# Kernel optimization log

Measured on AMD Instinct MI355X. Metric: run time of the kernel, lower is better.

## Reference

```python
import jax, jax.numpy as jnp
import numpy as np

N, L, E_Q, E_TOTAL, H, FORECAST = 4, 2048, 512, 512, 8, 8
E_HEAD = E_TOTAL // H
DT = 1.0
NEG = -1e30


def setup_inputs() -> dict:
    rng = jax.random.key(0)
    ks = jax.random.split(rng, 8)
    inv = 1.0 / np.sqrt(E_Q)
    return {
        "query": jax.random.normal(ks[0], (N, L, E_Q), jnp.float32),
        "key": jax.random.normal(ks[1], (N, L, E_Q), jnp.float32),
        "value": jax.random.normal(ks[2], (N, L, E_Q), jnp.float32),
        "Wqkv": jax.random.normal(ks[3], (E_Q, 3 * E_TOTAL), jnp.float32) * inv,
        "bqkv": jnp.zeros((3 * E_TOTAL,), jnp.float32),
        "Wo": jax.random.normal(ks[4], (E_TOTAL, E_Q), jnp.float32) * (1.0 / np.sqrt(E_TOTAL)),
        "bo": jnp.zeros((E_Q,), jnp.float32),
        "Xi": jax.random.normal(ks[5], (H, E_HEAD, E_HEAD), jnp.float32) * 0.02,
    }


def reference(query, key, value, Wqkv, bqkv, Wo, bo, Xi):
    # NOTE: original forward projects `query` into q,k,v (key/value args unused).
    b, s, _ = query.shape
    qkv = query @ Wqkv + bqkv                      # [b, s, 3E]
    q, k, v = jnp.split(qkv, 3, axis=-1)
    split_heads = lambda t: t.reshape(b, s, H, E_HEAD).transpose(0, 2, 1, 3)  # [b,H,s,h]
    q, k, v = split_heads(q), split_heads(k), split_heads(v)
    # causal SDPA
    scale = 1.0 / np.sqrt(E_HEAD)
    scores = jnp.einsum('bhqd,bhkd->bhqk', q, k) * scale
    causal = jnp.tril(jnp.ones((s, s), bool))
    scores = jnp.where(causal, scores, NEG)
    probs = jax.nn.softmax(scores, axis=-1)
    attn = jnp.einsum('bhqk,bhkd->bhqd', probs, v)  # [b,H,s,h]
    # per-head SINDy linear dynamics, strict symmetry -> skew-symmetric A
    A = Xi - jnp.swapaxes(Xi, -1, -2)               # [H,h,h]

    def step(x, _):
        x2 = x + DT * jnp.einsum('bhsd,hde->bhse', x, A)
        return x2, x2

    _, ys = jax.lax.scan(step, attn, None, length=FORECAST)  # [n,b,H,s,h]
    roll = jnp.transpose(ys, (1, 0, 3, 2, 4)).reshape(b, FORECAST, s, E_TOTAL)
    return roll @ Wo + bo                            # [b, n, s, E_q]
```

## Files before the change

kernel.cpp:

```cpp
#include <hip/hip_runtime.h>
#include <math.h>


#define NEGV -1e30f

typedef __bf16 bf16_t;
typedef __bf16 bf16x4 __attribute__((ext_vector_type(4)));
typedef __bf16 bf16x8 __attribute__((ext_vector_type(8)));
typedef float f32x4 __attribute__((ext_vector_type(4)));

#define MFMA(a, b, c) __builtin_amdgcn_mfma_f32_16x16x32_bf16((a), (b), (c), 0, 0, 0)

#define QSCALE 0.18033688011112042f

__device__ __forceinline__ bf16x8* swz_ptr(bf16_t* base, int r, int cb) {
  return (bf16x8*)((char*)base + r * 128 + (cb ^ ((r & 7) << 4)));
}
__device__ __forceinline__ const bf16x8* swz_cptr(const bf16_t* base, int r, int cb) {
  return (const bf16x8*)((const char*)base + r * 128 + (cb ^ ((r & 7) << 4)));
}

__global__ __launch_bounds__(256) void build_powers(const float* __restrict__ Xi,
                                                    float* __restrict__ pows) {
  const int h = blockIdx.x;
  __shared__ __align__(16) float P[64][68];
  __shared__ __align__(16) float cur[64][68];
  const int tid = threadIdx.x;
  const float* xi = Xi + (size_t)h * 4096;
  float* dst = pows + (size_t)h * 8 * 4096;
  for (int idx = tid; idx < 4096; idx += 256) {
    const int i = idx >> 6, j = idx & 63;
    const float p = (i == j ? 1.f : 0.f) + xi[i * 64 + j] - xi[j * 64 + i];
    P[i][j] = p;
    cur[i][j] = p;
    dst[idx] = p;
  }
  __syncthreads();
  const int i = tid >> 2;
  const int j0 = (tid & 3) * 16;
  for (int n = 1; n < 8; ++n) {
    float a[16];
#pragma unroll
    for (int jj = 0; jj < 16; ++jj) a[jj] = 0.f;
    for (int dd = 0; dd < 64; ++dd) {
      const float c = cur[i][dd];
#pragma unroll
      for (int jj = 0; jj < 16; ++jj) a[jj] += c * P[dd][j0 + jj];
    }
    __syncthreads();
#pragma unroll
    for (int jj = 0; jj < 16; ++jj) {
      cur[i][j0 + jj] = a[jj];
      dst[n * 4096 + i * 64 + j0 + jj] = a[jj];
    }
    __syncthreads();
  }
}

__global__ __launch_bounds__(256) void build_B(const float* __restrict__ pows,
                                               const float* __restrict__ Wo,
                                               bf16_t* __restrict__ BmatT) {
  const int et = blockIdx.x;
  const int n = blockIdx.y;
  const int h = blockIdx.z;
  __shared__ __align__(16) float P[64][68];
  __shared__ __align__(16) float We[64][128];
  const int tid = threadIdx.x;
  const float* src = pows + ((size_t)h * 8 + n) * 4096;
  for (int idx = tid; idx < 4096; idx += 256) P[idx >> 6][idx & 63] = src[idx];
  const int e0 = et * 128;
  for (int idx = tid; idx < 8192; idx += 256) {
    const int dd = idx >> 7, e = idx & 127;
    We[dd][e] = Wo[(size_t)(h * 64 + dd) * 512 + e0 + e];
  }
  __syncthreads();
  const int d = tid >> 2;
  const int eq = (tid & 3) * 32;
  float acc[32];
#pragma unroll
  for (int j = 0; j < 32; ++j) acc[j] = 0.f;
  for (int dd = 0; dd < 64; ++dd) {
    const float p = P[d][dd];
#pragma unroll
    for (int j = 0; j < 32; ++j) acc[j] += p * We[dd][eq + j];
  }
  bf16_t* dst = BmatT + (size_t)n * 512 * 512 + (size_t)(e0 + eq) * 512 + h * 64 + d;
#pragma unroll
  for (int j = 0; j < 32; ++j) dst[(size_t)j * 512] = (bf16_t)acc[j];
}

__global__ __launch_bounds__(256) void qkv_gemm(const float* __restrict__ X,
                                                const float* __restrict__ W,
                                                const float* __restrict__ bias,
                                                bf16_t* __restrict__ qw,
                                                bf16_t* __restrict__ kw,
                                                bf16_t* __restrict__ vt) {
  __shared__ __align__(16) bf16_t As[128][72];
  __shared__ __align__(16) bf16_t Bs[128][72];
  const int tid = threadIdx.x;
  const int wave = tid >> 6, lane = tid & 63;
  const int g = lane >> 4, li = lane & 15;
  const int row0 = blockIdx.x * 128;
  const int col0 = blockIdx.y * 128;
  const int wm = (wave >> 1) * 64, wn = (wave & 1) * 64;
  f32x4 acc[4][4] = {};
  const int m_st = tid >> 1;
  const int kh = (tid & 1) * 32;
  const int nl = tid & 127;
  const int kq = tid >> 7;
  for (int k0 = 0; k0 < 512; k0 += 64) {
    {
      const float* asrc = X + (size_t)(row0 + m_st) * 512 + k0 + kh;
#pragma unroll
      for (int c = 0; c < 4; ++c) {
        const float4 f0 = ((const float4*)asrc)[c * 2];
        const float4 f1 = ((const float4*)asrc)[c * 2 + 1];
        bf16x8 v;
        v[0] = (bf16_t)f0.x; v[1] = (bf16_t)f0.y; v[2] = (bf16_t)f0.z; v[3] = (bf16_t)f0.w;
        v[4] = (bf16_t)f1.x; v[5] = (bf16_t)f1.y; v[6] = (bf16_t)f1.z; v[7] = (bf16_t)f1.w;
        *(bf16x8*)&As[m_st][kh + c * 8] = v;
      }
      const float* bsrc = W + (size_t)(k0 + kq * 32) * 1536 + col0 + nl;
#pragma unroll
      for (int c = 0; c < 4; ++c) {
        bf16x8 v;
#pragma unroll
        for (int j = 0; j < 8; ++j) v[j] = (bf16_t)bsrc[(size_t)(c * 8 + j) * 1536];
        *(bf16x8*)&Bs[nl][kq * 32 + c * 8] = v;
      }
    }
    __syncthreads();
#pragma unroll
    for (int ks = 0; ks < 2; ++ks) {
      bf16x8 af[4], bfr[4];
#pragma unroll
      for (int mr = 0; mr < 4; ++mr)
        af[mr] = *(const bf16x8*)&As[wm + mr * 16 + li][ks * 32 + g * 8];
#pragma unroll
      for (int nr = 0; nr < 4; ++nr)
        bfr[nr] = *(const bf16x8*)&Bs[wn + nr * 16 + li][ks * 32 + g * 8];
#pragma unroll
      for (int mr = 0; mr < 4; ++mr)
#pragma unroll
        for (int nr = 0; nr < 4; ++nr)
          acc[mr][nr] = MFMA(af[mr], bfr[nr], acc[mr][nr]);
    }
    __syncthreads();
  }
  const int cbase = col0 + wn;
  const int sel = cbase >> 9;
  const int hh = (cbase & 511) >> 6;
  const int bb = row0 >> 11;
  const size_t hb = (size_t)(bb * 8 + hh) * (2048 * 64);
  if (sel == 2) {
    bf16_t* vbase = vt + hb;
#pragma unroll
    for (int nr = 0; nr < 4; ++nr) {
      const int dcol = nr * 16 + li;
      const float bv = bias[cbase + dcol];
#pragma unroll
      for (int mr = 0; mr < 4; ++mr) {
        bf16x4 pk;
#pragma unroll
        for (int i = 0; i < 4; ++i) pk[i] = (bf16_t)(acc[mr][nr][i] + bv);
        const int s = (row0 + wm + mr * 16 + g * 4) & 2047;
        *(bf16x4*)&vbase[(size_t)dcol * 2048 + s] = pk;
      }
    }
  } else {
    bf16_t* dstp = (sel == 0 ? qw : kw) + hb;
    const float sc = (sel == 0) ? QSCALE : 1.0f;
#pragma unroll
    for (int nr = 0; nr < 4; ++nr) {
      const int dcol = nr * 16 + li;
      const float bv = bias[cbase + dcol];
#pragma unroll
      for (int mr = 0; mr < 4; ++mr) {
#pragma unroll
        for (int i = 0; i < 4; ++i) {
          const int r = row0 + wm + mr * 16 + g * 4 + i;
          const int s = r & 2047;
          dstp[(size_t)s * 64 + dcol] = (bf16_t)((acc[mr][nr][i] + bv) * sc);
        }
      }
    }
  }
}

__global__ __launch_bounds__(256, 4) void fattn(const bf16_t* __restrict__ qw,
                                                const bf16_t* __restrict__ kw,
                                                const bf16_t* __restrict__ vt,
                                                bf16_t* __restrict__ attn) {
  __shared__ __align__(16) bf16_t Ks[2][64][64];
  __shared__ __align__(16) bf16_t Vs[2][64][64];
  __shared__ __align__(16) bf16_t Ps[4][16][64];
  const int tid = threadIdx.x;
  const int w = tid >> 6;
  const int lane = tid & 63;
  const int g = lane >> 4;
  const int li = lane & 15;
  const int qt = (int)gridDim.x - 1 - (int)blockIdx.x;
  const int h = blockIdx.y;
  const int b = blockIdx.z;
  const size_t base = ((size_t)(b * 8 + h)) * (2048 * 64);
  const int q0 = qt * 64;
  const int qrow = q0 + w * 16 + li;
  const bf16x8 aq0 = *(const bf16x8*)(qw + base + (size_t)qrow * 64 + g * 8);
  const bf16x8 aq1 = *(const bf16x8*)(qw + base + (size_t)qrow * 64 + 32 + g * 8);
  const bf16_t* kbase = kw + base;
  const bf16_t* vbase = vt + base;
  const int r_st = tid >> 2;
  const int qu = tid & 3;
  {
    const bf16_t* kp = kbase + (size_t)r_st * 64 + qu * 16;
    const bf16_t* vp = vbase + (size_t)r_st * 2048 + qu * 16;
    *swz_ptr(&Ks[0][0][0], r_st, qu * 32) = *(const bf16x8*)kp;
    *swz_ptr(&Ks[0][0][0], r_st, qu * 32 + 16) = *(const bf16x8*)(kp + 8);
    *swz_ptr(&Vs[0][0][0], r_st, qu * 32) = *(const bf16x8*)vp;
    *swz_ptr(&Vs[0][0][0], r_st, qu * 32 + 16) = *(const bf16x8*)(vp + 8);
  }
  f32x4 accO[4] = {};
  float m_run = -__builtin_inff();
  float l_run = 0.f;
  char* const psrow = (char*)&Ps[w][li][0];
  const int pswz = (li & 7) << 4;
  for (int kt = 0; kt <= qt; ++kt) {
    __syncthreads();
    const int cur = kt & 1;
    const bool pf = kt < qt;
    bf16x8 nk0, nk1, nv0, nv1;
    if (pf) {
      const int kb2 = (kt + 1) * 64;
      const bf16_t* kp = kbase + (size_t)(kb2 + r_st) * 64 + qu * 16;
      const bf16_t* vp = vbase + (size_t)r_st * 2048 + kb2 + qu * 16;
      nk0 = *(const bf16x8*)kp;
      nk1 = *(const bf16x8*)(kp + 8);
      nv0 = *(const bf16x8*)vp;
      nv1 = *(const bf16x8*)(vp + 8);
    }
    f32x4 sv[4];
    __builtin_amdgcn_s_setprio(1);
#pragma unroll
    for (int nt = 0; nt < 4; ++nt) {
      const bf16x8 bk0 = *swz_cptr(&Ks[cur][0][0], nt * 16 + li, g * 16);
      const bf16x8 bk1 = *swz_cptr(&Ks[cur][0][0], nt * 16 + li, 64 + g * 16);
      f32x4 z = {0.f, 0.f, 0.f, 0.f};
      z = MFMA(bk0, aq0, z);
      sv[nt] = MFMA(bk1, aq1, z);
    }
    __builtin_amdgcn_s_setprio(0);
    if (kt == qt) {
#pragma unroll
      for (int nt = 0; nt < 4; ++nt)
#pragma unroll
        for (int i = 0; i < 4; ++i)
          if (nt * 16 + g * 4 + i > w * 16 + li) sv[nt][i] = NEGV;
    }
    float pmax = sv[0][0];
#pragma unroll
    for (int nt = 0; nt < 4; ++nt)
#pragma unroll
      for (int i = 0; i < 4; ++i) pmax = fmaxf(pmax, sv[nt][i]);
    pmax = fmaxf(pmax, __shfl_xor(pmax, 16, 64));
    pmax = fmaxf(pmax, __shfl_xor(pmax, 32, 64));
    if (!__all(pmax - m_run <= 8.f)) {
      const float newm = fmaxf(m_run, pmax);
      const float sc = exp2f(m_run - newm);
      l_run *= sc;
      m_run = newm;
#pragma unroll
      for (int nt = 0; nt < 4; ++nt)
#pragma unroll
        for (int i = 0; i < 4; ++i) accO[nt][i] *= sc;
    }
    float rsum = 0.f;
#pragma unroll
    for (int nt = 0; nt < 4; ++nt) {
#pragma unroll
      for (int i = 0; i < 4; ++i) {
        const float p = exp2f(sv[nt][i] - m_run);
        sv[nt][i] = p;
        rsum += p;
      }
    }
    rsum += __shfl_xor(rsum, 16, 64);
    rsum += __shfl_xor(rsum, 32, 64);
    l_run += rsum;
#pragma unroll
    for (int nt = 0; nt < 4; ++nt) {
      bf16x4 pk;
#pragma unroll
      for (int i = 0; i < 4; ++i) pk[i] = (bf16_t)sv[nt][i];
      *(bf16x4*)(psrow + ((nt * 32 + g * 8) ^ pswz)) = pk;
    }
    const bf16x8 ap0 = *(const bf16x8*)(psrow + ((g * 16) ^ pswz));
    const bf16x8 ap1 = *(const bf16x8*)(psrow + ((64 + g * 16) ^ pswz));
    __builtin_amdgcn_s_setprio(1);
#pragma unroll
    for (int nt = 0; nt < 4; ++nt) {
      const bf16x8 bv0 = *swz_cptr(&Vs[cur][0][0], nt * 16 + li, g * 16);
      const bf16x8 bv1 = *swz_cptr(&Vs[cur][0][0], nt * 16 + li, 64 + g * 16);
      accO[nt] = MFMA(bv0, ap0, accO[nt]);
      accO[nt] = MFMA(bv1, ap1, accO[nt]);
    }
    __builtin_amdgcn_s_setprio(0);
    if (pf) {
      *swz_ptr(&Ks[cur ^ 1][0][0], r_st, qu * 32) = nk0;
      *swz_ptr(&Ks[cur ^ 1][0][0], r_st, qu * 32 + 16) = nk1;
      *swz_ptr(&Vs[cur ^ 1][0][0], r_st, qu * 32) = nv0;
      *swz_ptr(&Vs[cur ^ 1][0][0], r_st, qu * 32 + 16) = nv1;
    }
  }
  {
    const float inv = 1.0f / l_run;
    bf16_t* arow = attn + (size_t)(b * 2048 + qrow) * 512 + h * 64;
#pragma unroll
    for (int nt = 0; nt < 4; ++nt) {
      bf16x4 pk;
#pragma unroll
      for (int i = 0; i < 4; ++i) pk[i] = (bf16_t)(accO[nt][i] * inv);
      *(bf16x4*)&arow[nt * 16 + g * 4] = pk;
    }
  }
}

__global__ __launch_bounds__(256) void out_gemm(const bf16_t* __restrict__ A,
                                                const bf16_t* __restrict__ BmatT,
                                                const float* __restrict__ bo,
                                                float* __restrict__ out) {
  __shared__ __align__(16) bf16_t As[128][72];
  __shared__ __align__(16) bf16_t Bs[128][72];
  const int tid = threadIdx.x;
  const int wave = tid >> 6, lane = tid & 63;
  const int g = lane >> 4, li = lane & 15;
  const int row0 = blockIdx.x * 128;
  const int col0 = blockIdx.y * 128;
  const int nf = blockIdx.z;
  const bf16_t* BT = BmatT + (size_t)nf * 512 * 512;
  const int wm = (wave >> 1) * 64, wn = (wave & 1) * 64;
  f32x4 acc[4][4] = {};
  const int m_st = tid >> 1;
  const int kh = (tid & 1) * 32;
  for (int k0 = 0; k0 < 512; k0 += 64) {
    {
      const bf16x8* asrc = (const bf16x8*)(A + (size_t)(row0 + m_st) * 512 + k0 + kh);
#pragma unroll
      for (int c = 0; c < 4; ++c) *(bf16x8*)&As[m_st][kh + c * 8] = asrc[c];
      const bf16x8* bsrc = (const bf16x8*)(BT + (size_t)(col0 + m_st) * 512 + k0 + kh);
#pragma unroll
      for (int c = 0; c < 4; ++c) *(bf16x8*)&Bs[m_st][kh + c * 8] = bsrc[c];
    }
    __syncthreads();
#pragma unroll
    for (int ks = 0; ks < 2; ++ks) {
      bf16x8 af[4], bfr[4];
#pragma unroll
      for (int mr = 0; mr < 4; ++mr)
        af[mr] = *(const bf16x8*)&As[wm + mr * 16 + li][ks * 32 + g * 8];
#pragma unroll
      for (int nr = 0; nr < 4; ++nr)
        bfr[nr] = *(const bf16x8*)&Bs[wn + nr * 16 + li][ks * 32 + g * 8];
#pragma unroll
      for (int mr = 0; mr < 4; ++mr)
#pragma unroll
        for (int nr = 0; nr < 4; ++nr)
          acc[mr][nr] = MFMA(af[mr], bfr[nr], acc[mr][nr]);
    }
    __syncthreads();
  }
  const int bb = row0 >> 11;
  float* obase = out + ((size_t)(bb * 8 + nf)) * (2048 * 512);
#pragma unroll
  for (int nr = 0; nr < 4; ++nr) {
    const int c = col0 + wn + nr * 16 + li;
    const float bv = bo[c];
#pragma unroll
    for (int mr = 0; mr < 4; ++mr) {
#pragma unroll
      for (int i = 0; i < 4; ++i) {
        const int r = row0 + wm + mr * 16 + g * 4 + i;
        const int s = r & 2047;
        obase[(size_t)s * 512 + c] = acc[mr][nr][i] + bv;
      }
    }
  }
}

extern "C" void kernel_launch(void* const* d_in, const int* in_sizes, int n_in,
                              void* d_out, int out_size, void* d_ws, size_t ws_size,
                              hipStream_t stream) {
  const float* query = (const float*)d_in[0];
  const float* Wqkv = (const float*)d_in[3];
  const float* bqkv = (const float*)d_in[4];
  const float* Wo = (const float*)d_in[5];
  const float* bo = (const float*)d_in[6];
  const float* Xi = (const float*)d_in[7];
  float* out = (float*)d_out;

  char* ws = (char*)d_ws;
  bf16_t* qw = (bf16_t*)(ws + 0);
  bf16_t* kw = (bf16_t*)(ws + 8388608);
  bf16_t* vt = (bf16_t*)(ws + 16777216);
  bf16_t* attn = (bf16_t*)(ws + 25165824);
  bf16_t* BmatT = (bf16_t*)(ws + 33554432);
  float* pows = (float*)(ws + 37748736);

  build_powers<<<dim3(8), dim3(256), 0, stream>>>(Xi, pows);
  build_B<<<dim3(4, 8, 8), dim3(256), 0, stream>>>(pows, Wo, BmatT);
  qkv_gemm<<<dim3(64, 12), dim3(256), 0, stream>>>(query, Wqkv, bqkv, qw, kw, vt);
  fattn<<<dim3(32, 8, 4), dim3(256), 0, stream>>>(qw, kw, vt, attn);
  out_gemm<<<dim3(64, 4, 8), dim3(256), 0, stream>>>(attn, BmatT, bo, out);
}
```

Measured before the change: 219.2 us.

## Pre-convert GEMM operands to swizzled bf16 and stage via direct global-to-LDS loads

Adds two pre-pass kernels that convert the query activations and the transposed Wqkv weights to bf16 in an XOR-swizzled layout. The producers of the out-GEMM operands (build_B, fattn) now write that same swizzled layout. Both GEMMs then stage tiles with global_load_lds 16-byte direct copies into unpadded swizzled LDS, removing the register round trip, the in-loop fp32-to-bf16 conversion and the strided weight gathers. The cost is two extra launches and an extra pass over the input through workspace (Xb aliases the attn buffer, which works because of launch order).

```diff
diff --git a/kernel.cpp b/kernel.cpp
--- a/kernel.cpp
+++ b/kernel.cpp
@@ -18,6 +18,49 @@
 }
 __device__ __forceinline__ const bf16x8* swz_cptr(const bf16_t* base, int r, int cb) {
   return (const bf16x8*)((const char*)base + r * 128 + (cb ^ ((r & 7) << 4)));
+}
+
+__device__ __forceinline__ void gload16(const bf16_t* g, bf16_t* l) {
+  __builtin_amdgcn_global_load_lds(
+      (const __attribute__((address_space(1))) void*)g,
+      (__attribute__((address_space(3))) void*)l, 16, 0, 0);
+}
+
+
+__global__ __launch_bounds__(256) void xconv(const float* __restrict__ X,
+                                             bf16_t* __restrict__ Xb) {
+  const int gid = blockIdx.x * 256 + threadIdx.x;
+  const int s = gid >> 6, j = gid & 63;
+  const float4* src = (const float4*)(X + (size_t)s * 512 + j * 8);
+  const float4 f0 = src[0], f1 = src[1];
+  bf16x8 v;
+  v[0] = (bf16_t)f0.x; v[1] = (bf16_t)f0.y; v[2] = (bf16_t)f0.z; v[3] = (bf16_t)f0.w;
+  v[4] = (bf16_t)f1.x; v[5] = (bf16_t)f1.y; v[6] = (bf16_t)f1.z; v[7] = (bf16_t)f1.w;
+  *(bf16x8*)&Xb[(size_t)s * 512 + (j >> 3) * 64 + 8 * ((j & 7) ^ (s & 7))] = v;
+}
+
+__global__ __launch_bounds__(256) void wconv(const float* __restrict__ W,
+                                             bf16_t* __restrict__ WT) {
+  const int n0 = blockIdx.x * 64, k0 = blockIdx.y * 64;
+  __shared__ float Wf[64][65];
+  const int tid = threadIdx.x;
+#pragma unroll
+  for (int c = 0; c < 16; ++c) {
+    const int idx = tid + c * 256;
+    const int kk = idx >> 6, nn = idx & 63;
+    Wf[kk][nn] = W[(size_t)(k0 + kk) * 1536 + n0 + nn];
+  }
+  __syncthreads();
+  const int nr = tid >> 2;
+  const int jb = (tid & 3) * 2;
+#pragma unroll
+  for (int t = 0; t < 2; ++t) {
+    const int j = jb + t;
+    bf16x8 v;
+#pragma unroll
+    for (int i = 0; i < 8; ++i) v[i] = (bf16_t)Wf[j * 8 + i][nr];
+    *(bf16x8*)&WT[(size_t)(n0 + nr) * 512 + k0 + 8 * (j ^ (nr & 7))] = v;
+  }
 }
 
 __global__ __launch_bounds__(256) void build_powers(const float* __restrict__ Xi,
@@ -84,19 +127,21 @@
 #pragma unroll
     for (int j = 0; j < 32; ++j) acc[j] += p * We[dd][eq + j];
   }
-  bf16_t* dst = BmatT + (size_t)n * 512 * 512 + (size_t)(e0 + eq) * 512 + h * 64 + d;
-#pragma unroll
-  for (int j = 0; j < 32; ++j) dst[(size_t)j * 512] = (bf16_t)acc[j];
-}
-
-__global__ __launch_bounds__(256) void qkv_gemm(const float* __restrict__ X,
-                                                const float* __restrict__ W,
+  bf16_t* dst = BmatT + (size_t)n * 512 * 512 + (size_t)(e0 + eq) * 512 + h * 64;
+  const int dlo = d & 7, dhi = d >> 3;
+#pragma unroll
+  for (int j = 0; j < 32; ++j)
+    dst[(size_t)j * 512 + 8 * (dhi ^ (j & 7)) + dlo] = (bf16_t)acc[j];
+}
+
+__global__ __launch_bounds__(256) void qkv_gemm(const bf16_t* __restrict__ Xb,
+                                                const bf16_t* __restrict__ WT,
                                                 const float* __restrict__ bias,
                                                 bf16_t* __restrict__ qw,
                                                 bf16_t* __restrict__ kw,
                                                 bf16_t* __restrict__ vt) {
-  __shared__ __align__(16) bf16_t As[128][72];
-  __shared__ __align__(16) bf16_t Bs[128][72];
+  __shared__ __align__(16) bf16_t As[128 * 64];
+  __shared__ __align__(16) bf16_t Bs[128 * 64];
   const int tid = threadIdx.x;
   const int wave = tid >> 6, lane = tid & 63;
   const int g = lane >> 4, li = lane & 15;
@@ -104,30 +149,15 @@
   const int col0 = blockIdx.y * 128;
   const int wm = (wave >> 1) * 64, wn = (wave & 1) * 64;
   f32x4 acc[4][4] = {};
-  const int m_st = tid >> 1;
-  const int kh = (tid & 1) * 32;
-  const int nl = tid & 127;
-  const int kq = tid >> 7;
+  const bf16_t* asrc = Xb + (size_t)(row0 + wave * 32 + (lane >> 3)) * 512 + (lane & 7) * 8;
+  const bf16_t* bsrc = WT + (size_t)(col0 + wave * 32 + (lane >> 3)) * 512 + (lane & 7) * 8;
+  bf16_t* adst = &As[wave * 32 * 64];
+  bf16_t* bdst = &Bs[wave * 32 * 64];
   for (int k0 = 0; k0 < 512; k0 += 64) {
-    {
-      const float* asrc = X + (size_t)(row0 + m_st) * 512 + k0 + kh;
-#pragma unroll
-      for (int c = 0; c < 4; ++c) {
-        const float4 f0 = ((const float4*)asrc)[c * 2];
-        const float4 f1 = ((const float4*)asrc)[c * 2 + 1];
-        bf16x8 v;
-        v[0] = (bf16_t)f0.x; v[1] = (bf16_t)f0.y; v[2] = (bf16_t)f0.z; v[3] = (bf16_t)f0.w;
-        v[4] = (bf16_t)f1.x; v[5] = (bf16_t)f1.y; v[6] = (bf16_t)f1.z; v[7] = (bf16_t)f1.w;
-        *(bf16x8*)&As[m_st][kh + c * 8] = v;
-      }
-      const float* bsrc = W + (size_t)(k0 + kq * 32) * 1536 + col0 + nl;
-#pragma unroll
-      for (int c = 0; c < 4; ++c) {
-        bf16x8 v;
-#pragma unroll
-        for (int j = 0; j < 8; ++j) v[j] = (bf16_t)bsrc[(size_t)(c * 8 + j) * 1536];
-        *(bf16x8*)&Bs[nl][kq * 32 + c * 8] = v;
-      }
+#pragma unroll
+    for (int c = 0; c < 4; ++c) {
+      gload16(asrc + (size_t)c * 8 * 512 + k0, adst + c * 512);
+      gload16(bsrc + (size_t)c * 8 * 512 + k0, bdst + c * 512);
     }
     __syncthreads();
 #pragma unroll
@@ -135,10 +165,10 @@
       bf16x8 af[4], bfr[4];
 #pragma unroll
       for (int mr = 0; mr < 4; ++mr)
-        af[mr] = *(const bf16x8*)&As[wm + mr * 16 + li][ks * 32 + g * 8];
+        af[mr] = *swz_cptr(As, wm + mr * 16 + li, ks * 64 + g * 16);
 #pragma unroll
       for (int nr = 0; nr < 4; ++nr)
-        bfr[nr] = *(const bf16x8*)&Bs[wn + nr * 16 + li][ks * 32 + g * 8];
+        bfr[nr] = *swz_cptr(Bs, wn + nr * 16 + li, ks * 64 + g * 16);
 #pragma unroll
       for (int mr = 0; mr < 4; ++mr)
 #pragma unroll
@@ -319,7 +349,7 @@
       bf16x4 pk;
 #pragma unroll
       for (int i = 0; i < 4; ++i) pk[i] = (bf16_t)(accO[nt][i] * inv);
-      *(bf16x4*)&arow[nt * 16 + g * 4] = pk;
+      *(bf16x4*)&arow[8 * ((nt * 2 + (g >> 1)) ^ (li & 7)) + (g & 1) * 4] = pk;
     }
   }
 }
@@ -328,27 +358,26 @@
                                                 const bf16_t* __restrict__ BmatT,
                                                 const float* __restrict__ bo,
                                                 float* __restrict__ out) {
-  __shared__ __align__(16) bf16_t As[128][72];
-  __shared__ __align__(16) bf16_t Bs[128][72];
+  __shared__ __align__(16) bf16_t As[128 * 64];
+  __shared__ __align__(16) bf16_t Bs[128 * 64];
   const int tid = threadIdx.x;
   const int wave = tid >> 6, lane = tid & 63;
   const int g = lane >> 4, li = lane & 15;
   const int row0 = blockIdx.x * 128;
   const int col0 = blockIdx.y * 128;
   const int nf = blockIdx.z;
-  const bf16_t* BT = BmatT + (size_t)nf * 512 * 512;
   const int wm = (wave >> 1) * 64, wn = (wave & 1) * 64;
   f32x4 acc[4][4] = {};
-  const int m_st = tid >> 1;
-  const int kh = (tid & 1) * 32;
+  const bf16_t* asrc = A + (size_t)(row0 + wave * 32 + (lane >> 3)) * 512 + (lane & 7) * 8;
+  const bf16_t* bsrc = BmatT + (size_t)nf * 512 * 512 +
+                       (size_t)(col0 + wave * 32 + (lane >> 3)) * 512 + (lane & 7) * 8;
+  bf16_t* adst = &As[wave * 32 * 64];
+  bf16_t* bdst = &Bs[wave * 32 * 64];
   for (int k0 = 0; k0 < 512; k0 += 64) {
-    {
-      const bf16x8* asrc = (const bf16x8*)(A + (size_t)(row0 + m_st) * 512 + k0 + kh);
-#pragma unroll
-      for (int c = 0; c < 4; ++c) *(bf16x8*)&As[m_st][kh + c * 8] = asrc[c];
-      const bf16x8* bsrc = (const bf16x8*)(BT + (size_t)(col0 + m_st) * 512 + k0 + kh);
-#pragma unroll
-      for (int c = 0; c < 4; ++c) *(bf16x8*)&Bs[m_st][kh + c * 8] = bsrc[c];
+#pragma unroll
+    for (int c = 0; c < 4; ++c) {
+      gload16(asrc + (size_t)c * 8 * 512 + k0, adst + c * 512);
+      gload16(bsrc + (size_t)c * 8 * 512 + k0, bdst + c * 512);
     }
     __syncthreads();
 #pragma unroll
@@ -356,10 +385,10 @@
       bf16x8 af[4], bfr[4];
 #pragma unroll
       for (int mr = 0; mr < 4; ++mr)
-        af[mr] = *(const bf16x8*)&As[wm + mr * 16 + li][ks * 32 + g * 8];
+        af[mr] = *swz_cptr(As, wm + mr * 16 + li, ks * 64 + g * 16);
 #pragma unroll
       for (int nr = 0; nr < 4; ++nr)
-        bfr[nr] = *(const bf16x8*)&Bs[wn + nr * 16 + li][ks * 32 + g * 8];
+        bfr[nr] = *swz_cptr(Bs, wn + nr * 16 + li, ks * 64 + g * 16);
 #pragma unroll
       for (int mr = 0; mr < 4; ++mr)
 #pragma unroll
@@ -401,13 +430,17 @@
   bf16_t* qw = (bf16_t*)(ws + 0);
   bf16_t* kw = (bf16_t*)(ws + 8388608);
   bf16_t* vt = (bf16_t*)(ws + 16777216);
+  bf16_t* Xb = (bf16_t*)(ws + 25165824);
   bf16_t* attn = (bf16_t*)(ws + 25165824);
   bf16_t* BmatT = (bf16_t*)(ws + 33554432);
   float* pows = (float*)(ws + 37748736);
-
+  bf16_t* WT = (bf16_t*)(ws + 38797312);
+
+  xconv<<<dim3(2048), dim3(256), 0, stream>>>(query, Xb);
+  wconv<<<dim3(24, 8), dim3(256), 0, stream>>>(Wqkv, WT);
   build_powers<<<dim3(8), dim3(256), 0, stream>>>(Xi, pows);
   build_B<<<dim3(4, 8, 8), dim3(256), 0, stream>>>(pows, Wo, BmatT);
-  qkv_gemm<<<dim3(64, 12), dim3(256), 0, stream>>>(query, Wqkv, bqkv, qw, kw, vt);
+  qkv_gemm<<<dim3(64, 12), dim3(256), 0, stream>>>(Xb, WT, bqkv, qw, kw, vt);
   fattn<<<dim3(32, 8, 4), dim3(256), 0, stream>>>(qw, kw, vt, attn);
   out_gemm<<<dim3(64, 4, 8), dim3(256), 0, stream>>>(attn, BmatT, bo, out);
 }
```

New measurement: 190.0 us. 1.15x faster.
